# Performance work log

Hardware: AMD Instinct MI355X
Metric: run time of the kernel (lower is better)

The kernel has to match this reference:

```python
import jax, jax.numpy as jnp
import numpy as np

E, T = 200000, 1500000
H, INT, BE, NR, NS = 128, 64, 8, 6, 7
N_BEFORE, N_AFTER = 1, 2


def _w(key, fan_in, fan_out):
    return jax.random.normal(key, (fan_in, fan_out), dtype=jnp.float32) / np.sqrt(fan_in)


def setup_inputs() -> dict:
    key = jax.random.key(0)
    ks = jax.random.split(key, 24)
    inp = {
        "x": jax.random.normal(ks[0], (E, H), dtype=jnp.float32),
        "rbf": jax.random.uniform(ks[1], (E, NR), dtype=jnp.float32),
        "sbf": jax.random.uniform(ks[2], (T, NS * NR), dtype=jnp.float32),
        "idx_kj": jax.random.randint(ks[3], (T,), 0, E),
        "idx_ji": jax.random.randint(ks[4], (T,), 0, E),
        # basis projections (no bias)
        "W_rbf1": _w(ks[5], NR, BE),
        "W_rbf2": _w(ks[6], BE, H),
        "W_sbf1": _w(ks[7], NS * NR, BE),
        "W_sbf2": _w(ks[8], BE, INT),
        # message transforms
        "W_kj": _w(ks[9], H, H),
        "b_kj": jnp.zeros((H,), dtype=jnp.float32),
        "W_ji": _w(ks[10], H, H),
        "b_ji": jnp.zeros((H,), dtype=jnp.float32),
        "W_down": _w(ks[11], H, INT),
        "W_up": _w(ks[12], INT, H),
        # residual layers before skip: [n, 2, H, H]
        "W_before": jax.random.normal(ks[13], (N_BEFORE, 2, H, H), dtype=jnp.float32) / np.sqrt(H),
        "b_before": jnp.zeros((N_BEFORE, 2, H), dtype=jnp.float32),
        "W_lin": _w(ks[14], H, H),
        "b_lin": jnp.zeros((H,), dtype=jnp.float32),
        "W_after": jax.random.normal(ks[15], (N_AFTER, 2, H, H), dtype=jnp.float32) / np.sqrt(H),
        "b_after": jnp.zeros((N_AFTER, 2, H), dtype=jnp.float32),
    }
    return inp


def reference(x, rbf, sbf, idx_kj, idx_ji, W_rbf1, W_rbf2, W_sbf1, W_sbf2,
              W_kj, b_kj, W_ji, b_ji, W_down, W_up,
              W_before, b_before, W_lin, b_lin, W_after, b_after):
    act = jax.nn.silu  # swish

    x_ji = act(x @ W_ji + b_ji)                       # [E, H]
    x_kj = act(x @ W_kj + b_kj)                       # [E, H]

    rbf_p = (rbf @ W_rbf1) @ W_rbf2                   # [E, H]
    x_kj = x_kj * rbf_p
    x_kj = act(x_kj @ W_down)                         # [E, INT]

    sbf_p = (sbf @ W_sbf1) @ W_sbf2                   # [T, INT]
    m = x_kj[idx_kj] * sbf_p                          # gather -> [T, INT]
    agg = jax.ops.segment_sum(m, idx_ji, num_segments=x.shape[0])  # [E, INT]
    x_kj = act(agg @ W_up)                            # [E, H]

    h = x_ji + x_kj
    for i in range(W_before.shape[0]):
        h = h + act(act(h @ W_before[i, 0] + b_before[i, 0]) @ W_before[i, 1] + b_before[i, 1])
    h = act(h @ W_lin + b_lin) + x
    for i in range(W_after.shape[0]):
        h = h + act(act(h @ W_after[i, 0] + b_after[i, 0]) @ W_after[i, 1] + b_after[i, 1])
    return h
```

## Files before the change

### kernel.cpp

```cpp
#include <hip/hip_runtime.h>

#define EN 200000
#define TN 1500000
#define NCHUNK ((TN + 63) >> 6)
#define SCAN_BLK 512
#define NB ((EN + SCAN_BLK - 1) / SCAN_BLK)

typedef short s16x8 __attribute__((ext_vector_type(8)));
typedef float f32x4 __attribute__((ext_vector_type(4)));

#define WJI   0
#define WKJ   16384
#define WDOWN 32768
#define WUP   40960
#define WB0   49152
#define WB1   65536
#define WLIN  81920
#define WA00  98304
#define WA01  114688
#define WA10  131072
#define WA11  147456
#define WSBFP 163840
#define WP_COUNT 167936

__device__ __forceinline__ unsigned short f2bf(float f) {
    unsigned int r;
    asm("v_cvt_pk_bf16_f32 %0, %1, %1" : "=v"(r) : "v"(f));
    return (unsigned short)r;
}
__device__ __forceinline__ float bf2f(unsigned short u) {
    return __uint_as_float(((unsigned int)u) << 16);
}
__device__ __forceinline__ float silu_f(float v) {
    return v * __builtin_amdgcn_rcpf(1.f + __expf(-v));
}

#define MFMA(a, b, c) __builtin_amdgcn_mfma_f32_16x16x32_bf16((a), (b), (c), 0, 0, 0)

__global__ void k_prep1(const float* __restrict__ Wr1, const float* __restrict__ Wr2,
                        const float* __restrict__ Ws1, const float* __restrict__ Ws2,
                        float* __restrict__ wrbfc, float* __restrict__ wsbfc) {
    int idx = blockIdx.x * 256 + threadIdx.x;
    if (idx < 768) {
        int r = idx >> 7, c = idx & 127;
        float s = 0.f;
        #pragma unroll
        for (int m = 0; m < 8; m++) s += Wr1[r * 8 + m] * Wr2[m * 128 + c];
        wrbfc[idx] = s;
    }
    int i2 = idx - 768;
    if (i2 >= 0 && i2 < 2688) {
        int r = i2 >> 6, c = i2 & 63;
        float s = 0.f;
        #pragma unroll
        for (int m = 0; m < 8; m++) s += Ws1[r * 8 + m] * Ws2[m * 64 + c];
        wsbfc[i2] = s;
    }
}

__global__ void k_prep2(const float* __restrict__ Wji, const float* __restrict__ Wkj,
                        const float* __restrict__ Wdown, const float* __restrict__ Wup,
                        const float* __restrict__ Wbef, const float* __restrict__ Wlin,
                        const float* __restrict__ Waft, const float* __restrict__ wsbfc,
                        unsigned short* __restrict__ wp) {
    for (int idx = blockIdx.x * 256 + threadIdx.x; idx < WP_COUNT; idx += gridDim.x * 256) {
        const float* src;
        int off, N;
        bool pad42 = false;
        if (idx < WKJ)        { src = Wji;           off = WJI;   N = 128; }
        else if (idx < WDOWN) { src = Wkj;           off = WKJ;   N = 128; }
        else if (idx < WUP)   { src = Wdown;         off = WDOWN; N = 64;  }
        else if (idx < WB0)   { src = Wup;           off = WUP;   N = 128; }
        else if (idx < WB1)   { src = Wbef;          off = WB0;   N = 128; }
        else if (idx < WLIN)  { src = Wbef + 16384;  off = WB1;   N = 128; }
        else if (idx < WA00)  { src = Wlin;          off = WLIN;  N = 128; }
        else if (idx < WA01)  { src = Waft;          off = WA00;  N = 128; }
        else if (idx < WA10)  { src = Waft + 16384;  off = WA01;  N = 128; }
        else if (idx < WA11)  { src = Waft + 32768;  off = WA10;  N = 128; }
        else if (idx < WSBFP) { src = Waft + 49152;  off = WA11;  N = 128; }
        else                  { src = wsbfc;         off = WSBFP; N = 64; pad42 = true; }
        int li = idx - off;
        int j = li & 7, lane = (li >> 3) & 63, rest = li >> 9;
        int ncb = N >> 4;
        int cb = rest % ncb, ks = rest / ncb;
        int k = ks * 32 + ((lane >> 4) << 3) + j;
        int n = cb * 16 + (lane & 15);
        float v = 0.f;
        if (!pad42 || k < 42) v = src[k * N + n];
        wp[idx] = f2bf(v);
    }
}

__global__ __launch_bounds__(256, 4) void k_edge1(
        const float* __restrict__ x, const float* __restrict__ rbf,
        const float* __restrict__ bkj, const float* __restrict__ bji,
        const unsigned short* __restrict__ wp, const float* __restrict__ wrbfc,
        float* __restrict__ xji, unsigned short* __restrict__ xd) {
    __shared__ unsigned short xa[64 * 136];
    __shared__ unsigned short kjt[64 * 136];
    const int tid = threadIdx.x;
    const int row0 = blockIdx.x * 64;
    {
        const float4* src = (const float4*)(x + (size_t)row0 * 128);
        #pragma unroll
        for (int k = 0; k < 8; k++) {
            int idx = tid + k * 256;
            float4 v = src[idx];
            int flat = idx << 2, r = flat >> 7, c = flat & 127;
            ushort4 u; u.x = f2bf(v.x); u.y = f2bf(v.y); u.z = f2bf(v.z); u.w = f2bf(v.w);
            *(ushort4*)&xa[r * 136 + c] = u;
        }
    }
    #pragma unroll
    for (int k = 0; k < 32; k++) {
        int idx = tid + k * 256;
        int r = idx >> 7, c = idx & 127;
        const float* rb = rbf + (size_t)(row0 + r) * 6;
        float s = rb[0] * wrbfc[c] + rb[1] * wrbfc[128 + c] + rb[2] * wrbfc[256 + c]
                + rb[3] * wrbfc[384 + c] + rb[4] * wrbfc[512 + c] + rb[5] * wrbfc[640 + c];
        kjt[r * 136 + c] = f2bf(s);
    }
    __syncthreads();
    const int w = tid >> 6, l = tid & 63, l15 = l & 15, l4 = l >> 4;
    s16x8 af[4];
    {
        const unsigned short* ab = &xa[(w * 16 + l15) * 136 + l4 * 8];
        #pragma unroll
        for (int ks = 0; ks < 4; ks++) af[ks] = *(const s16x8*)(ab + ks * 32);
    }
    #pragma unroll
    for (int cb = 0; cb < 8; cb++) {
        f32x4 accj = {0.f, 0.f, 0.f, 0.f};
        f32x4 acck = {0.f, 0.f, 0.f, 0.f};
        #pragma unroll
        for (int ks = 0; ks < 4; ks++) {
            s16x8 bfj = *(const s16x8*)(wp + WJI + (((ks << 3) + cb) * 64 + l) * 8);
            s16x8 bfk = *(const s16x8*)(wp + WKJ + (((ks << 3) + cb) * 64 + l) * 8);
            accj = MFMA(af[ks], bfj, accj);
            acck = MFMA(af[ks], bfk, acck);
        }
        int col = (cb << 4) + l15;
        float bvj = bji[col];
        float bvk = bkj[col];
        #pragma unroll
        for (int i = 0; i < 4; i++) {
            int r = w * 16 + l4 * 4 + i;
            xji[(size_t)(row0 + r) * 128 + col] = silu_f(accj[i] + bvj);
            float rp = bf2f(kjt[r * 136 + col]);
            kjt[r * 136 + col] = f2bf(silu_f(acck[i] + bvk) * rp);
        }
    }
    __syncthreads();
    s16x8 ag[4];
    {
        const unsigned short* ab = &kjt[(w * 16 + l15) * 136 + l4 * 8];
        #pragma unroll
        for (int ks = 0; ks < 4; ks++) ag[ks] = *(const s16x8*)(ab + ks * 32);
    }
    #pragma unroll
    for (int cb = 0; cb < 4; cb++) {
        f32x4 acc = {0.f, 0.f, 0.f, 0.f};
        #pragma unroll
        for (int ks = 0; ks < 4; ks++) {
            s16x8 bf = *(const s16x8*)(wp + WDOWN + (((ks << 2) + cb) * 64 + l) * 8);
            acc = MFMA(ag[ks], bf, acc);
        }
        int col = (cb << 4) + l15;
        #pragma unroll
        for (int i = 0; i < 4; i++) {
            int r = w * 16 + l4 * 4 + i;
            xd[(size_t)(row0 + r) * 64 + col] = f2bf(silu_f(acc[i]));
        }
    }
}

__global__ void k_hist(const int* __restrict__ iji, int* __restrict__ cnt) {
    for (int t = blockIdx.x * 256 + threadIdx.x; t < TN; t += gridDim.x * 256)
        atomicAdd(&cnt[iji[t]], 1);
}

__global__ __launch_bounds__(SCAN_BLK) void k_scan1(const int* __restrict__ cnt, int* __restrict__ bsum) {
    __shared__ int s[SCAN_BLK];
    int i = threadIdx.x, gi = blockIdx.x * SCAN_BLK + i;
    s[i] = (gi < EN) ? cnt[gi] : 0;
    __syncthreads();
    for (int d = SCAN_BLK >> 1; d > 0; d >>= 1) {
        if (i < d) s[i] += s[i + d];
        __syncthreads();
    }
    if (i == 0) bsum[blockIdx.x] = s[0];
}

__global__ __launch_bounds__(SCAN_BLK) void k_scan2(const int* __restrict__ bsum, int* __restrict__ bscan) {
    __shared__ int s[SCAN_BLK];
    int i = threadIdx.x;
    int v = (i < NB) ? bsum[i] : 0;
    s[i] = v;
    __syncthreads();
    for (int d = 1; d < SCAN_BLK; d <<= 1) {
        int t = (i >= d) ? s[i - d] : 0;
        __syncthreads();
        s[i] += t;
        __syncthreads();
    }
    if (i < NB) bscan[i] = s[i] - v;
}

__global__ __launch_bounds__(SCAN_BLK) void k_scan3(const int* __restrict__ cnt, const int* __restrict__ bscan,
                                                    int* __restrict__ segoff, int* __restrict__ cursor) {
    __shared__ int s[SCAN_BLK];
    int i = threadIdx.x, gi = blockIdx.x * SCAN_BLK + i;
    int c = (gi < EN) ? cnt[gi] : 0;
    s[i] = c;
    __syncthreads();
    for (int d = 1; d < SCAN_BLK; d <<= 1) {
        int t = (i >= d) ? s[i - d] : 0;
        __syncthreads();
        s[i] += t;
        __syncthreads();
    }
    int off = bscan[blockIdx.x] + s[i] - c;
    if (gi < EN) { segoff[gi] = off; cursor[gi] = off; }
    if (blockIdx.x == 0 && i == 0) segoff[EN] = TN;
}

__global__ void k_rank(const int* __restrict__ iji, int* __restrict__ cursor, int* __restrict__ pos) {
    for (int t = blockIdx.x * 256 + threadIdx.x; t < TN; t += gridDim.x * 256)
        pos[t] = atomicAdd(&cursor[iji[t]], 1);
}

__global__ __launch_bounds__(256) void k_mscat(
        const float* __restrict__ sbf, const int* __restrict__ ikj, const int* __restrict__ pos,
        const unsigned short* __restrict__ wp, const unsigned short* __restrict__ xd,
        unsigned short* __restrict__ msort) {
    __shared__ unsigned short sb[64 * 72];
    const int tid = threadIdx.x;
    const int w = tid >> 6, l = tid & 63, l15 = l & 15, l4 = l >> 4;
    for (int idx = tid; idx < 64 * 72; idx += 256) sb[idx] = 0;
    __syncthreads();
    for (int ch = blockIdx.x; ch < NCHUNK; ch += gridDim.x) {
        const int t0 = ch << 6;
        const int nt = min(64, TN - t0);
        const int tot = nt * 42;
        const float* src = sbf + (size_t)t0 * 42;
        for (int idx = tid; idx < tot; idx += 256) {
            int r = idx / 42, c = idx - r * 42;
            sb[r * 72 + c] = f2bf(src[idx]);
        }
        __syncthreads();
        s16x8 afr[2];
        {
            const unsigned short* ab = &sb[(w * 16 + l15) * 72 + l4 * 8];
            afr[0] = *(const s16x8*)ab;
            afr[1] = *(const s16x8*)(ab + 32);
        }
        f32x4 accs[4];
        #pragma unroll
        for (int cb = 0; cb < 4; cb++) {
            f32x4 acc = {0.f, 0.f, 0.f, 0.f};
            acc = MFMA(afr[0], *(const s16x8*)(wp + WSBFP + ((cb) * 64 + l) * 8), acc);
            acc = MFMA(afr[1], *(const s16x8*)(wp + WSBFP + ((4 + cb) * 64 + l) * 8), acc);
            accs[cb] = acc;
        }
        #pragma unroll
        for (int i = 0; i < 4; i++) {
            int r = w * 16 + l4 * 4 + i;
            if (r < nt) {
                int t = t0 + r;
                int a = ikj[t];
                size_t mb = (size_t)pos[t] * 64;
                const unsigned short* xr = xd + (size_t)a * 64;
                #pragma unroll
                for (int cb = 0; cb < 4; cb++) {
                    int col = (cb << 4) + l15;
                    msort[mb + col] = f2bf(accs[cb][i] * bf2f(xr[col]));
                }
            }
        }
        __syncthreads();
    }
}

__global__ __launch_bounds__(256) void k_seg(
        const unsigned short* __restrict__ msort, const int* __restrict__ segoff,
        float* __restrict__ agg) {
    int e = blockIdx.x * 4 + (threadIdx.x >> 6);
    if (e >= EN) return;
    int l = threadIdx.x & 63;
    int sub = l >> 5, c2 = l & 31;
    int n0 = segoff[e], n1 = segoff[e + 1];
    float a0 = 0.f, a1 = 0.f;
    for (int p = n0 + sub; p < n1; p += 2) {
        unsigned int u = *(const unsigned int*)(msort + (size_t)p * 64 + c2 * 2);
        a0 += bf2f((unsigned short)(u & 0xFFFF));
        a1 += bf2f((unsigned short)(u >> 16));
    }
    a0 += __shfl_xor(a0, 32, 64);
    a1 += __shfl_xor(a1, 32, 64);
    if (sub == 0) {
        float2 o = {a0, a1};
        *(float2*)(agg + (size_t)e * 64 + c2 * 2) = o;
    }
}

__global__ __launch_bounds__(256) void k_trip(
        const float* __restrict__ sbf, const int* __restrict__ ikj, const int* __restrict__ iji,
        const unsigned short* __restrict__ wp, const unsigned short* __restrict__ xd,
        float* __restrict__ agg) {
    __shared__ unsigned short sb[64 * 72];
    const int tid = threadIdx.x;
    const int w = tid >> 6, l = tid & 63, l15 = l & 15, l4 = l >> 4;
    for (int idx = tid; idx < 64 * 72; idx += 256) sb[idx] = 0;
    __syncthreads();
    for (int ch = blockIdx.x; ch < NCHUNK; ch += gridDim.x) {
        const int t0 = ch << 6;
        const int nt = min(64, TN - t0);
        const int tot = nt * 42;
        const float* src = sbf + (size_t)t0 * 42;
        for (int idx = tid; idx < tot; idx += 256) {
            int r = idx / 42, c = idx - r * 42;
            sb[r * 72 + c] = f2bf(src[idx]);
        }
        __syncthreads();
        s16x8 afr[2];
        {
            const unsigned short* ab = &sb[(w * 16 + l15) * 72 + l4 * 8];
            afr[0] = *(const s16x8*)ab;
            afr[1] = *(const s16x8*)(ab + 32);
        }
        #pragma unroll
        for (int cb = 0; cb < 4; cb++) {
            f32x4 acc = {0.f, 0.f, 0.f, 0.f};
            acc = MFMA(afr[0], *(const s16x8*)(wp + WSBFP + ((cb) * 64 + l) * 8), acc);
            acc = MFMA(afr[1], *(const s16x8*)(wp + WSBFP + ((4 + cb) * 64 + l) * 8), acc);
            int col = (cb << 4) + l15;
            #pragma unroll
            for (int i = 0; i < 4; i++) {
                int r = w * 16 + l4 * 4 + i;
                if (r < nt) {
                    int t = t0 + r;
                    int a = ikj[t], g = iji[t];
                    float m = acc[i] * bf2f(xd[(size_t)a * 64 + col]);
                    atomicAdd(&agg[(size_t)g * 64 + col], m);
                }
            }
        }
        __syncthreads();
    }
}

__device__ __forceinline__ void layer_reg(float (*h)[4], unsigned short* s0, unsigned short* s1,
                                          const unsigned short* wp0, const float* b0,
                                          const unsigned short* wp1, const float* b1,
                                          int w, int l, int l15, int l4) {
    #pragma unroll
    for (int cb = 0; cb < 8; cb++) {
        int col = (cb << 4) + l15;
        #pragma unroll
        for (int i = 0; i < 4; i++)
            s0[((w << 4) + (l4 << 2) + i) * 136 + col] = f2bf(h[cb][i]);
    }
    __syncthreads();
    {
        const unsigned short* ab = &s0[((w << 4) + l15) * 136 + (l4 << 3)];
        s16x8 a0 = *(const s16x8*)ab, a1 = *(const s16x8*)(ab + 32);
        s16x8 a2 = *(const s16x8*)(ab + 64), a3 = *(const s16x8*)(ab + 96);
        #pragma unroll
        for (int cb = 0; cb < 8; cb++) {
            f32x4 acc = {0.f, 0.f, 0.f, 0.f};
            acc = MFMA(a0, *(const s16x8*)(wp0 + ((cb) * 64 + l) * 8), acc);
            acc = MFMA(a1, *(const s16x8*)(wp0 + ((8 + cb) * 64 + l) * 8), acc);
            acc = MFMA(a2, *(const s16x8*)(wp0 + ((16 + cb) * 64 + l) * 8), acc);
            acc = MFMA(a3, *(const s16x8*)(wp0 + ((24 + cb) * 64 + l) * 8), acc);
            int col = (cb << 4) + l15;
            float bv = b0[col];
            #pragma unroll
            for (int i = 0; i < 4; i++)
                s1[((w << 4) + (l4 << 2) + i) * 136 + col] = f2bf(silu_f(acc[i] + bv));
        }
    }
    __syncthreads();
    {
        const unsigned short* ab = &s1[((w << 4) + l15) * 136 + (l4 << 3)];
        s16x8 a0 = *(const s16x8*)ab, a1 = *(const s16x8*)(ab + 32);
        s16x8 a2 = *(const s16x8*)(ab + 64), a3 = *(const s16x8*)(ab + 96);
        #pragma unroll
        for (int cb = 0; cb < 8; cb++) {
            f32x4 acc = {0.f, 0.f, 0.f, 0.f};
            acc = MFMA(a0, *(const s16x8*)(wp1 + ((cb) * 64 + l) * 8), acc);
            acc = MFMA(a1, *(const s16x8*)(wp1 + ((8 + cb) * 64 + l) * 8), acc);
            acc = MFMA(a2, *(const s16x8*)(wp1 + ((16 + cb) * 64 + l) * 8), acc);
            acc = MFMA(a3, *(const s16x8*)(wp1 + ((24 + cb) * 64 + l) * 8), acc);
            int col = (cb << 4) + l15;
            float bv = b1[col];
            #pragma unroll
            for (int i = 0; i < 4; i++) h[cb][i] += silu_f(acc[i] + bv);
        }
    }
    __syncthreads();
}

__global__ __launch_bounds__(256, 4) void k_edge2(
        const float* __restrict__ agg, const float* __restrict__ x,
        const unsigned short* __restrict__ wp, const float* __restrict__ bbef,
        const float* __restrict__ blin, const float* __restrict__ baft,
        float* __restrict__ out) {
    __shared__ unsigned short aa[64 * 136];
    __shared__ unsigned short bb[64 * 136];
    const int tid = threadIdx.x;
    const int row0 = blockIdx.x * 64;
    const int w = tid >> 6, l = tid & 63, l15 = l & 15, l4 = l >> 4;
    {
        const float4* src = (const float4*)(agg + (size_t)row0 * 64);
        #pragma unroll
        for (int k = 0; k < 4; k++) {
            int idx = tid + k * 256;
            float4 v = src[idx];
            int flat = idx << 2, r = flat >> 6, c = flat & 63;
            ushort4 u; u.x = f2bf(v.x); u.y = f2bf(v.y); u.z = f2bf(v.z); u.w = f2bf(v.w);
            *(ushort4*)&aa[r * 72 + c] = u;
        }
    }
    float h[8][4];
    #pragma unroll
    for (int cb = 0; cb < 8; cb++) {
        int col = (cb << 4) + l15;
        #pragma unroll
        for (int i = 0; i < 4; i++) {
            int r = (w << 4) + (l4 << 2) + i;
            h[cb][i] = out[(size_t)(row0 + r) * 128 + col];
        }
    }
    __syncthreads();
    {
        const unsigned short* ab = &aa[((w << 4) + l15) * 72 + (l4 << 3)];
        s16x8 a0 = *(const s16x8*)ab, a1 = *(const s16x8*)(ab + 32);
        #pragma unroll
        for (int cb = 0; cb < 8; cb++) {
            f32x4 acc = {0.f, 0.f, 0.f, 0.f};
            acc = MFMA(a0, *(const s16x8*)(wp + WUP + ((cb) * 64 + l) * 8), acc);
            acc = MFMA(a1, *(const s16x8*)(wp + WUP + ((8 + cb) * 64 + l) * 8), acc);
            #pragma unroll
            for (int i = 0; i < 4; i++) h[cb][i] += silu_f(acc[i]);
        }
    }
    __syncthreads();
    layer_reg(h, bb, aa, wp + WB0, bbef, wp + WB1, bbef + 128, w, l, l15, l4);
    #pragma unroll
    for (int cb = 0; cb < 8; cb++) {
        int col = (cb << 4) + l15;
        #pragma unroll
        for (int i = 0; i < 4; i++)
            bb[((w << 4) + (l4 << 2) + i) * 136 + col] = f2bf(h[cb][i]);
    }
    __syncthreads();
    {
        const unsigned short* ab = &bb[((w << 4) + l15) * 136 + (l4 << 3)];
        s16x8 a0 = *(const s16x8*)ab, a1 = *(const s16x8*)(ab + 32);
        s16x8 a2 = *(const s16x8*)(ab + 64), a3 = *(const s16x8*)(ab + 96);
        #pragma unroll
        for (int cb = 0; cb < 8; cb++) {
            f32x4 acc = {0.f, 0.f, 0.f, 0.f};
            acc = MFMA(a0, *(const s16x8*)(wp + WLIN + ((cb) * 64 + l) * 8), acc);
            acc = MFMA(a1, *(const s16x8*)(wp + WLIN + ((8 + cb) * 64 + l) * 8), acc);
            acc = MFMA(a2, *(const s16x8*)(wp + WLIN + ((16 + cb) * 64 + l) * 8), acc);
            acc = MFMA(a3, *(const s16x8*)(wp + WLIN + ((24 + cb) * 64 + l) * 8), acc);
            int col = (cb << 4) + l15;
            float bv = blin[col];
            #pragma unroll
            for (int i = 0; i < 4; i++) {
                int r = (w << 4) + (l4 << 2) + i;
                h[cb][i] = silu_f(acc[i] + bv) + x[(size_t)(row0 + r) * 128 + col];
            }
        }
    }
    __syncthreads();
    layer_reg(h, aa, bb, wp + WA00, baft, wp + WA01, baft + 128, w, l, l15, l4);
    layer_reg(h, aa, bb, wp + WA10, baft + 256, wp + WA11, baft + 384, w, l, l15, l4);
    #pragma unroll
    for (int cb = 0; cb < 8; cb++) {
        int col = (cb << 4) + l15;
        #pragma unroll
        for (int i = 0; i < 4; i++) {
            int r = (w << 4) + (l4 << 2) + i;
            out[(size_t)(row0 + r) * 128 + col] = h[cb][i];
        }
    }
}

extern "C" void kernel_launch(void* const* d_in, const int* in_sizes, int n_in,
                              void* d_out, int out_size, void* d_ws, size_t ws_size,
                              hipStream_t stream) {
    const float* x     = (const float*)d_in[0];
    const float* rbf   = (const float*)d_in[1];
    const float* sbf   = (const float*)d_in[2];
    const int*   ikj   = (const int*)d_in[3];
    const int*   iji   = (const int*)d_in[4];
    const float* Wr1   = (const float*)d_in[5];
    const float* Wr2   = (const float*)d_in[6];
    const float* Ws1   = (const float*)d_in[7];
    const float* Ws2   = (const float*)d_in[8];
    const float* Wkj   = (const float*)d_in[9];
    const float* bkj   = (const float*)d_in[10];
    const float* Wji   = (const float*)d_in[11];
    const float* bji   = (const float*)d_in[12];
    const float* Wdown = (const float*)d_in[13];
    const float* Wup   = (const float*)d_in[14];
    const float* Wbef  = (const float*)d_in[15];
    const float* bbef  = (const float*)d_in[16];
    const float* Wlin  = (const float*)d_in[17];
    const float* blin  = (const float*)d_in[18];
    const float* Waft  = (const float*)d_in[19];
    const float* baft  = (const float*)d_in[20];

    char* ws = (char*)d_ws;
    size_t o = 0;
    auto alloc = [&](size_t bytes) { size_t r = o; o = (o + bytes + 255) & ~(size_t)255; return r; };
    size_t o_agg   = alloc((size_t)EN * 64 * 4);
    size_t o_xd    = alloc((size_t)EN * 64 * 2);
    size_t o_wp    = alloc((size_t)WP_COUNT * 2);
    size_t o_wrbfc = alloc(768 * 4);
    size_t o_wsbfc = alloc(2688 * 4);
    size_t o_cnt   = alloc((size_t)EN * 4);
    size_t o_soff  = alloc((size_t)(EN + 1) * 4);
    size_t o_cur   = alloc((size_t)EN * 4);
    size_t o_bsum  = alloc(SCAN_BLK * 4);
    size_t o_bscan = alloc(SCAN_BLK * 4);
    size_t o_pos   = alloc((size_t)TN * 4);
    size_t o_msort = alloc((size_t)TN * 64 * 2);
    size_t need_sorted = o;

    float* agg          = (float*)(ws + o_agg);
    unsigned short* xd  = (unsigned short*)(ws + o_xd);
    unsigned short* wp  = (unsigned short*)(ws + o_wp);
    float* wrbfc        = (float*)(ws + o_wrbfc);
    float* wsbfc        = (float*)(ws + o_wsbfc);
    int* cnt            = (int*)(ws + o_cnt);
    int* segoff         = (int*)(ws + o_soff);
    int* cursor         = (int*)(ws + o_cur);
    int* bsum           = (int*)(ws + o_bsum);
    int* bscan          = (int*)(ws + o_bscan);
    int* pos            = (int*)(ws + o_pos);
    unsigned short* msort = (unsigned short*)(ws + o_msort);
    float* out          = (float*)d_out;

    k_prep1<<<14, 256, 0, stream>>>(Wr1, Wr2, Ws1, Ws2, wrbfc, wsbfc);
    k_prep2<<<656, 256, 0, stream>>>(Wji, Wkj, Wdown, Wup, Wbef, Wlin, Waft, wsbfc, wp);
    k_edge1<<<EN / 64, 256, 0, stream>>>(x, rbf, bkj, bji, wp, wrbfc, out, xd);

    if (ws_size >= need_sorted) {
        hipMemsetAsync(cnt, 0, (size_t)EN * 4, stream);
        k_hist<<<2048, 256, 0, stream>>>(iji, cnt);
        k_scan1<<<NB, SCAN_BLK, 0, stream>>>(cnt, bsum);
        k_scan2<<<1, SCAN_BLK, 0, stream>>>(bsum, bscan);
        k_scan3<<<NB, SCAN_BLK, 0, stream>>>(cnt, bscan, segoff, cursor);
        k_rank<<<2048, 256, 0, stream>>>(iji, cursor, pos);
        k_mscat<<<4096, 256, 0, stream>>>(sbf, ikj, pos, wp, xd, msort);
        k_seg<<<(EN + 3) / 4, 256, 0, stream>>>(msort, segoff, agg);
    } else {
        hipMemsetAsync(agg, 0, (size_t)EN * 64 * 4, stream);
        k_trip<<<4096, 256, 0, stream>>>(sbf, ikj, iji, wp, xd, agg);
    }

    k_edge2<<<EN / 64, 256, 0, stream>>>(agg, x, wp, bbef, blin, baft, out);
}
```

Before: 678.0 us.

## Fuse message compute with segment reduction over sorted triplet order

Instead of computing messages in input order and scattering a bf16 message array into sorted positions for a separate segment-sum kernel, the rank kernel now writes a sorted permutation and sorted ikj indices. A fused kernel processes 64 sorted triplets per block: it gathers sbf rows through the permutation, runs the MFMA projection, multiplies by the gathered xd rows into shared memory, and reduces segments locally. Segments fully inside a chunk are stored directly and boundary segments use atomics. This removes the TN×64 bf16 intermediate write and read-back, but sbf rows are now read in gathered rather than streaming order, and it adds a binary-search kernel plus a memset of agg.

```diff
diff --git a/kernel.cpp b/kernel.cpp
--- a/kernel.cpp
+++ b/kernel.cpp
@@ -224,82 +224,88 @@
     if (blockIdx.x == 0 && i == 0) segoff[EN] = TN;
 }
 
-__global__ void k_rank(const int* __restrict__ iji, int* __restrict__ cursor, int* __restrict__ pos) {
-    for (int t = blockIdx.x * 256 + threadIdx.x; t < TN; t += gridDim.x * 256)
-        pos[t] = atomicAdd(&cursor[iji[t]], 1);
-}
-
-__global__ __launch_bounds__(256) void k_mscat(
-        const float* __restrict__ sbf, const int* __restrict__ ikj, const int* __restrict__ pos,
-        const unsigned short* __restrict__ wp, const unsigned short* __restrict__ xd,
-        unsigned short* __restrict__ msort) {
+__global__ void k_rank(const int* __restrict__ iji, const int* __restrict__ ikj,
+                       int* __restrict__ cursor, int* __restrict__ sortidx,
+                       int* __restrict__ ikjs) {
+    for (int t = blockIdx.x * 256 + threadIdx.x; t < TN; t += gridDim.x * 256) {
+        int p = atomicAdd(&cursor[iji[t]], 1);
+        sortidx[p] = t;
+        ikjs[p] = ikj[t];
+    }
+}
+
+__global__ void k_e0map(const int* __restrict__ segoff, int* __restrict__ e0map) {
+    int c = blockIdx.x * 256 + threadIdx.x;
+    if (c >= NCHUNK) return;
+    int p0 = c << 6;
+    int lo = 0, hi = EN - 1;
+    while (lo < hi) {
+        int mid = (lo + hi) >> 1;
+        if (segoff[mid + 1] > p0) hi = mid; else lo = mid + 1;
+    }
+    e0map[c] = lo;
+}
+
+__global__ __launch_bounds__(256) void k_mseg(
+        const float* __restrict__ sbf, const int* __restrict__ sortidx,
+        const int* __restrict__ ikjs, const unsigned short* __restrict__ wp,
+        const unsigned short* __restrict__ xd, const int* __restrict__ segoff,
+        const int* __restrict__ e0map, float* __restrict__ agg) {
+    __shared__ int tl[64];
     __shared__ unsigned short sb[64 * 72];
+    __shared__ float mt[64 * 66];
     const int tid = threadIdx.x;
+    const int ch = blockIdx.x;
+    const int p0 = ch << 6;
+    const int nt = min(64, TN - p0);
+    if (tid < 64) tl[tid] = (tid < nt) ? sortidx[p0 + tid] : 0;
+    __syncthreads();
+    for (int idx = tid; idx < 64 * 72; idx += 256) {
+        int r = idx / 72, c = idx - r * 72;
+        unsigned short v = 0;
+        if (c < 42 && r < nt) v = f2bf(sbf[(size_t)tl[r] * 42 + c]);
+        sb[idx] = v;
+    }
+    __syncthreads();
     const int w = tid >> 6, l = tid & 63, l15 = l & 15, l4 = l >> 4;
-    for (int idx = tid; idx < 64 * 72; idx += 256) sb[idx] = 0;
-    __syncthreads();
-    for (int ch = blockIdx.x; ch < NCHUNK; ch += gridDim.x) {
-        const int t0 = ch << 6;
-        const int nt = min(64, TN - t0);
-        const int tot = nt * 42;
-        const float* src = sbf + (size_t)t0 * 42;
-        for (int idx = tid; idx < tot; idx += 256) {
-            int r = idx / 42, c = idx - r * 42;
-            sb[r * 72 + c] = f2bf(src[idx]);
-        }
-        __syncthreads();
-        s16x8 afr[2];
-        {
-            const unsigned short* ab = &sb[(w * 16 + l15) * 72 + l4 * 8];
-            afr[0] = *(const s16x8*)ab;
-            afr[1] = *(const s16x8*)(ab + 32);
-        }
-        f32x4 accs[4];
+    s16x8 afr[2];
+    {
+        const unsigned short* ab = &sb[(w * 16 + l15) * 72 + l4 * 8];
+        afr[0] = *(const s16x8*)ab;
+        afr[1] = *(const s16x8*)(ab + 32);
+    }
+    f32x4 accs[4];
+    #pragma unroll
+    for (int cb = 0; cb < 4; cb++) {
+        f32x4 acc = {0.f, 0.f, 0.f, 0.f};
+        acc = MFMA(afr[0], *(const s16x8*)(wp + WSBFP + ((cb) * 64 + l) * 8), acc);
+        acc = MFMA(afr[1], *(const s16x8*)(wp + WSBFP + ((4 + cb) * 64 + l) * 8), acc);
+        accs[cb] = acc;
+    }
+    #pragma unroll
+    for (int i = 0; i < 4; i++) {
+        int r = w * 16 + l4 * 4 + i;
+        int a = (r < nt) ? ikjs[p0 + r] : 0;
+        const unsigned short* xr = xd + (size_t)a * 64;
         #pragma unroll
         for (int cb = 0; cb < 4; cb++) {
-            f32x4 acc = {0.f, 0.f, 0.f, 0.f};
-            acc = MFMA(afr[0], *(const s16x8*)(wp + WSBFP + ((cb) * 64 + l) * 8), acc);
-            acc = MFMA(afr[1], *(const s16x8*)(wp + WSBFP + ((4 + cb) * 64 + l) * 8), acc);
-            accs[cb] = acc;
-        }
-        #pragma unroll
-        for (int i = 0; i < 4; i++) {
-            int r = w * 16 + l4 * 4 + i;
-            if (r < nt) {
-                int t = t0 + r;
-                int a = ikj[t];
-                size_t mb = (size_t)pos[t] * 64;
-                const unsigned short* xr = xd + (size_t)a * 64;
-                #pragma unroll
-                for (int cb = 0; cb < 4; cb++) {
-                    int col = (cb << 4) + l15;
-                    msort[mb + col] = f2bf(accs[cb][i] * bf2f(xr[col]));
-                }
-            }
-        }
-        __syncthreads();
-    }
-}
-
-__global__ __launch_bounds__(256) void k_seg(
-        const unsigned short* __restrict__ msort, const int* __restrict__ segoff,
-        float* __restrict__ agg) {
-    int e = blockIdx.x * 4 + (threadIdx.x >> 6);
-    if (e >= EN) return;
-    int l = threadIdx.x & 63;
-    int sub = l >> 5, c2 = l & 31;
-    int n0 = segoff[e], n1 = segoff[e + 1];
-    float a0 = 0.f, a1 = 0.f;
-    for (int p = n0 + sub; p < n1; p += 2) {
-        unsigned int u = *(const unsigned int*)(msort + (size_t)p * 64 + c2 * 2);
-        a0 += bf2f((unsigned short)(u & 0xFFFF));
-        a1 += bf2f((unsigned short)(u >> 16));
-    }
-    a0 += __shfl_xor(a0, 32, 64);
-    a1 += __shfl_xor(a1, 32, 64);
-    if (sub == 0) {
-        float2 o = {a0, a1};
-        *(float2*)(agg + (size_t)e * 64 + c2 * 2) = o;
+            int col = (cb << 4) + l15;
+            mt[r * 66 + col] = accs[cb][i] * bf2f(xr[col]);
+        }
+    }
+    __syncthreads();
+    const int p1 = p0 + nt;
+    for (int e = e0map[ch] + w; e < EN; e += 4) {
+        int s0 = segoff[e];
+        if (s0 >= p1) break;
+        int s1 = segoff[e + 1];
+        int n0 = max(s0 - p0, 0);
+        int n1 = min(s1 - p0, nt);
+        float sum = 0.f;
+        for (int q = n0; q < n1; q++) sum += mt[q * 66 + l];
+        bool interior = (s0 >= p0) && (s1 <= p1);
+        if (interior) agg[(size_t)e * 64 + l] = sum;
+        else if (n1 > n0) atomicAdd(&agg[(size_t)e * 64 + l], sum);
     }
 }
 
@@ -526,8 +532,9 @@
     size_t o_cur   = alloc((size_t)EN * 4);
     size_t o_bsum  = alloc(SCAN_BLK * 4);
     size_t o_bscan = alloc(SCAN_BLK * 4);
-    size_t o_pos   = alloc((size_t)TN * 4);
-    size_t o_msort = alloc((size_t)TN * 64 * 2);
+    size_t o_sidx  = alloc((size_t)TN * 4);
+    size_t o_ikjs  = alloc((size_t)TN * 4);
+    size_t o_e0    = alloc((size_t)NCHUNK * 4);
     size_t need_sorted = o;
 
     float* agg          = (float*)(ws + o_agg);
@@ -540,8 +547,9 @@
     int* cursor         = (int*)(ws + o_cur);
     int* bsum           = (int*)(ws + o_bsum);
     int* bscan          = (int*)(ws + o_bscan);
-    int* pos            = (int*)(ws + o_pos);
-    unsigned short* msort = (unsigned short*)(ws + o_msort);
+    int* sortidx        = (int*)(ws + o_sidx);
+    int* ikjs           = (int*)(ws + o_ikjs);
+    int* e0map          = (int*)(ws + o_e0);
     float* out          = (float*)d_out;
 
     k_prep1<<<14, 256, 0, stream>>>(Wr1, Wr2, Ws1, Ws2, wrbfc, wsbfc);
@@ -554,9 +562,10 @@
         k_scan1<<<NB, SCAN_BLK, 0, stream>>>(cnt, bsum);
         k_scan2<<<1, SCAN_BLK, 0, stream>>>(bsum, bscan);
         k_scan3<<<NB, SCAN_BLK, 0, stream>>>(cnt, bscan, segoff, cursor);
-        k_rank<<<2048, 256, 0, stream>>>(iji, cursor, pos);
-        k_mscat<<<4096, 256, 0, stream>>>(sbf, ikj, pos, wp, xd, msort);
-        k_seg<<<(EN + 3) / 4, 256, 0, stream>>>(msort, segoff, agg);
+        k_rank<<<2048, 256, 0, stream>>>(iji, ikj, cursor, sortidx, ikjs);
+        k_e0map<<<(NCHUNK + 255) / 256, 256, 0, stream>>>(segoff, e0map);
+        hipMemsetAsync(agg, 0, (size_t)EN * 64 * 4, stream);
+        k_mseg<<<NCHUNK, 256, 0, stream>>>(sbf, sortidx, ikjs, wp, xd, segoff, e0map, agg);
     } else {
         hipMemsetAsync(agg, 0, (size_t)EN * 64 * 4, stream);
         k_trip<<<4096, 256, 0, stream>>>(sbf, ikj, iji, wp, xd, agg);
```

Result: slower. 736.9 us (+8.7%).
